# Kernel optimization log

Hardware: AMD Instinct MI355X
Metric: run time of the kernel (lower is better)

Reference implementation:

```python
import jax, jax.numpy as jnp
import numpy as np

D_MODEL = 256
NHEAD = 8
D_HEAD = D_MODEL // NHEAD


def setup_inputs() -> dict:
    key = jax.random.key(0)
    ks = jax.random.split(key, 5)
    s = 0.02
    return {
        "x": jax.random.normal(ks[0], (2, 4096, D_MODEL), dtype=jnp.float32),
        "source": jax.random.normal(ks[1], (2, 6144, D_MODEL), dtype=jnp.float32),
        "Wq": jax.random.normal(ks[2], (D_MODEL, D_MODEL), dtype=jnp.float32) * s,
        "Wk": jax.random.normal(ks[3], (D_MODEL, D_MODEL), dtype=jnp.float32) * s,
        "Wv": jax.random.normal(ks[4], (D_MODEL, D_MODEL), dtype=jnp.float32) * s,
    }


def reference(x, source, Wq, Wk, Wv):
    B, L1, D = x.shape
    L2 = source.shape[1]
    scale = D_HEAD ** (-0.5)
    # torch Linear: y = x @ W.T  (W is [out, in])
    q = (x @ Wq.T).reshape(B, L1, NHEAD, D_HEAD)
    k = (source @ Wk.T).reshape(B, L2, NHEAD, D_HEAD)
    v = (source @ Wv.T).reshape(B, L2, NHEAD, D_HEAD)
    # scores: [B, H, L1, L2]
    attn = jnp.einsum("bqhd,bkhd->bhqk", q, k) * scale
    attn = jax.nn.softmax(attn, axis=-1)
    out = jnp.einsum("bhqk,bkhd->bqhd", attn, v)
    return out.reshape(B, L1, D)
```

## Files before the change

### kernel.cpp

```cpp
#include <hip/hip_runtime.h>
#include <math.h>

#define B_   2
#define L1_  4096
#define L2_  6144
#define DM_  256
#define H_   8
#define DH_  32

typedef __bf16 bf16x8 __attribute__((ext_vector_type(8)));
typedef __bf16 bf16x4 __attribute__((ext_vector_type(4)));
typedef float floatx4 __attribute__((ext_vector_type(4)));

__device__ __forceinline__ bf16x8 ldb(const __bf16* p) { return *(const bf16x8*)p; }

__device__ __forceinline__ bf16x4 pack4(floatx4 v) {
    bf16x4 r;
    r[0] = (__bf16)v[0]; r[1] = (__bf16)v[1];
    r[2] = (__bf16)v[2]; r[3] = (__bf16)v[3];
    return r;
}

__device__ inline bf16x8 load_cvt8(const float* __restrict__ p, float scale) {
    float4 a = *(const float4*)p;
    float4 b = *(const float4*)(p + 4);
    bf16x8 r;
    r[0] = (__bf16)(a.x * scale); r[1] = (__bf16)(a.y * scale);
    r[2] = (__bf16)(a.z * scale); r[3] = (__bf16)(a.w * scale);
    r[4] = (__bf16)(b.x * scale); r[5] = (__bf16)(b.y * scale);
    r[6] = (__bf16)(b.z * scale); r[7] = (__bf16)(b.w * scale);
    return r;
}

__global__ __launch_bounds__(256) void cvtW_kernel(
    const float* __restrict__ wq, const float* __restrict__ wk,
    const float* __restrict__ wv, __bf16* __restrict__ o, float qscale)
{
    int i = blockIdx.x * 256 + threadIdx.x;
    int seg = i >> 14;
    int off = (i & 16383) * 4;
    const float* src = seg == 0 ? wq : (seg == 1 ? wk : wv);
    float s = seg == 0 ? qscale : 1.0f;
    float4 v = *(const float4*)(src + off);
    __bf16* dst = o + (size_t)seg * 65536 + off;
    dst[0] = (__bf16)(v.x * s); dst[1] = (__bf16)(v.y * s);
    dst[2] = (__bf16)(v.z * s); dst[3] = (__bf16)(v.w * s);
}

template<bool WBF>
__global__ __launch_bounds__(256, 2) void proj_kernel(
    const float* __restrict__ x, const float* __restrict__ src,
    const float* __restrict__ Wqf, const float* __restrict__ Wkf, const float* __restrict__ Wvf,
    const __bf16* __restrict__ Wbf,
    __bf16* __restrict__ qo, __bf16* __restrict__ ko, __bf16* __restrict__ vo,
    float qscale)
{
    const int y = blockIdx.y;
    const int L = (y == 0) ? L1_ : L2_;
    if (blockIdx.x * 32 >= B_ * L) return;

    const float*  X   = (y == 0) ? x : src;
    const float*  Wf  = (y == 0) ? Wqf : (y == 1 ? Wkf : Wvf);
    const __bf16* Wb  = Wbf + (size_t)y * 65536;
    __bf16*       out = (y == 0) ? qo : (y == 1 ? ko : vo);
    const float   ascale = (!WBF && y == 0) ? qscale : 1.0f;

    const int lane = threadIdx.x & 63;
    const int w    = threadIdx.x >> 6;
    const int g    = lane >> 4;
    const int c    = lane & 15;
    const int mb   = blockIdx.x * 32;
    const int b    = mb / L;
    const int lb   = mb - b * L;

    floatx4 acc[2][4];
#pragma unroll
    for (int s = 0; s < 2; s++)
#pragma unroll
        for (int n = 0; n < 4; n++) acc[s][n] = (floatx4){0.f, 0.f, 0.f, 0.f};

#pragma unroll
    for (int kc = 0; kc < 8; kc++) {
        bf16x8 xf0 = load_cvt8(X + (size_t)(mb + c) * DM_ + kc * 32 + g * 8, ascale);
        bf16x8 xf1 = load_cvt8(X + (size_t)(mb + 16 + c) * DM_ + kc * 32 + g * 8, ascale);
#pragma unroll
        for (int n = 0; n < 4; n++) {
            const int oc = w * 64 + n * 16 + c;
            bf16x8 wf;
            if (WBF) wf = ldb(Wb + (size_t)oc * DM_ + kc * 32 + g * 8);
            else     wf = load_cvt8(Wf + (size_t)oc * DM_ + kc * 32 + g * 8, 1.0f);
            if (y == 2) {
                acc[0][n] = __builtin_amdgcn_mfma_f32_16x16x32_bf16(xf0, wf, acc[0][n], 0, 0, 0);
                acc[1][n] = __builtin_amdgcn_mfma_f32_16x16x32_bf16(xf1, wf, acc[1][n], 0, 0, 0);
            } else {
                acc[0][n] = __builtin_amdgcn_mfma_f32_16x16x32_bf16(wf, xf0, acc[0][n], 0, 0, 0);
                acc[1][n] = __builtin_amdgcn_mfma_f32_16x16x32_bf16(wf, xf1, acc[1][n], 0, 0, 0);
            }
        }
    }

    const int bhb = b * H_;
    if (y == 2) {
#pragma unroll
        for (int s = 0; s < 2; s++)
#pragma unroll
            for (int n = 0; n < 4; n++) {
                int d = (n & 1) * 16 + c;
                int h = w * 2 + (n >> 1);
                int l = lb + s * 16 + g * 4;
                *(bf16x4*)(out + ((size_t)(bhb + h) * DH_ + d) * (size_t)L + l) = pack4(acc[s][n]);
            }
    } else {
#pragma unroll
        for (int s = 0; s < 2; s++)
#pragma unroll
            for (int n = 0; n < 4; n++) {
                int dlo = (n & 1) * 16 + g * 4;
                int h = w * 2 + (n >> 1);
                int l = lb + s * 16 + c;
                *(bf16x4*)(out + ((size_t)(bhb + h) * (size_t)L + l) * DH_ + dlo) = pack4(acc[s][n]);
            }
    }
}

__device__ __forceinline__ void attn_step(
    const bf16x8 (&qf)[4], const bf16x8 (&kf)[4], bf16x8 (&kfN)[4],
    const __bf16* __restrict__ knext,
    const __bf16* __restrict__ vb0, const __bf16* __restrict__ vb1, int kb,
    __bf16* __restrict__ Pw, int g, int c,
    float (&l)[4], floatx4 (&o)[4][2])
{
    bf16x8 vf0 = ldb(vb0 + kb);
    bf16x8 vf1 = ldb(vb1 + kb);
    bf16x8 vf2 = ldb(vb0 + kb + 32);
    bf16x8 vf3 = ldb(vb1 + kb + 32);
    kfN[0] = ldb(knext);
    kfN[1] = ldb(knext + 16 * DH_);
    kfN[2] = ldb(knext + 32 * DH_);
    kfN[3] = ldb(knext + 48 * DH_);

#pragma unroll
    for (int h = 0; h < 4; h++) {
        floatx4 s[4];
#pragma unroll
        for (int st = 0; st < 4; st++)
            s[st] = __builtin_amdgcn_mfma_f32_16x16x32_bf16(
                        kf[st], qf[h], (floatx4){0.f, 0.f, 0.f, 0.f}, 0, 0, 0);
#pragma unroll
        for (int st = 0; st < 4; st++) {
            float a0 = __builtin_amdgcn_exp2f(s[st][0]);
            float a1 = __builtin_amdgcn_exp2f(s[st][1]);
            float a2 = __builtin_amdgcn_exp2f(s[st][2]);
            float a3 = __builtin_amdgcn_exp2f(s[st][3]);
            l[h] += (a0 + a1) + (a2 + a3);
            bf16x4 pk;
            pk[0] = (__bf16)a0; pk[1] = (__bf16)a1;
            pk[2] = (__bf16)a2; pk[3] = (__bf16)a3;
            *(bf16x4*)(Pw + h * 1024 + ((st * 2 + (g >> 1)) * 16 + c) * 8 + (g & 1) * 4) = pk;
        }
    }

#pragma unroll
    for (int kc = 0; kc < 2; kc++) {
#pragma unroll
        for (int h = 0; h < 4; h++) {
            bf16x8 pa = *(const bf16x8*)(Pw + h * 1024 + ((kc * 4 + g) * 16 + c) * 8);
            o[h][0] = __builtin_amdgcn_mfma_f32_16x16x32_bf16(pa, kc ? vf2 : vf0, o[h][0], 0, 0, 0);
            o[h][1] = __builtin_amdgcn_mfma_f32_16x16x32_bf16(pa, kc ? vf3 : vf1, o[h][1], 0, 0, 0);
        }
    }
}

template<bool DIRECT>
__global__ __launch_bounds__(256, 2) void attn_kernel(
    const __bf16* __restrict__ Q, const __bf16* __restrict__ K,
    const __bf16* __restrict__ VT, float* __restrict__ out,
    float* __restrict__ Opart, float* __restrict__ Lpart, int klen)
{
    __shared__ __bf16 ldsP[4][4][1024];

    const int lane  = threadIdx.x & 63;
    const int w     = threadIdx.x >> 6;
    const int g     = lane >> 4;
    const int c     = lane & 15;
    const int qbase = blockIdx.x * 256 + w * 64;
    const int bh    = blockIdx.y;
    const int k0    = blockIdx.z * klen;

    bf16x8 qf[4];
#pragma unroll
    for (int h = 0; h < 4; h++)
        qf[h] = ldb(Q + ((size_t)bh * L1_ + qbase + h * 16 + c) * DH_ + g * 8);

    const __bf16* kbase = K  + (size_t)bh * L2_ * DH_ + (size_t)c * DH_ + g * 8;
    const __bf16* vb0   = VT + ((size_t)bh * DH_ + c)      * L2_ + g * 8;
    const __bf16* vb1   = VT + ((size_t)bh * DH_ + 16 + c) * L2_ + g * 8;
    __bf16* Pw = &ldsP[w][0][0];

    float l[4] = {0.f, 0.f, 0.f, 0.f};
    floatx4 o[4][2];
#pragma unroll
    for (int h = 0; h < 4; h++) { o[h][0] = (floatx4){0.f,0.f,0.f,0.f}; o[h][1] = (floatx4){0.f,0.f,0.f,0.f}; }

    bf16x8 kfA[4], kfB[4];
#pragma unroll
    for (int st = 0; st < 4; st++)
        kfA[st] = ldb(kbase + (size_t)(k0 + st * 16) * DH_);

    for (int t = 0; t < klen; t += 128) {
        int kb = k0 + t;
        attn_step(qf, kfA, kfB, kbase + (size_t)(kb + 64) * DH_,
                  vb0, vb1, kb, Pw, g, c, l, o);
        int nn = (t + 128 < klen) ? kb + 128 : k0;
        attn_step(qf, kfB, kfA, kbase + (size_t)nn * DH_,
                  vb0, vb1, kb + 64, Pw, g, c, l, o);
    }

#pragma unroll
    for (int h = 0; h < 4; h++) {
        l[h] += __shfl_xor(l[h], 16, 64);
        l[h] += __shfl_xor(l[h], 32, 64);
    }

    const int b  = bh / H_;
    const int hh = bh % H_;
    if (DIRECT) {
#pragma unroll
        for (int h = 0; h < 4; h++)
#pragma unroll
            for (int r = 0; r < 4; r++) {
                float lr  = __shfl(l[h], g * 4 + r, 64);
                float inv = 1.0f / lr;
                size_t base = ((size_t)(b * L1_ + qbase + h * 16 + g * 4 + r)) * DM_ + hh * DH_;
                out[base + c]      = o[h][0][r] * inv;
                out[base + 16 + c] = o[h][1][r] * inv;
            }
    } else {
        float* Op = Opart + (size_t)blockIdx.z * ((size_t)B_ * L1_ * DM_);
#pragma unroll
        for (int h = 0; h < 4; h++) {
#pragma unroll
            for (int r = 0; r < 4; r++) {
                size_t base = ((size_t)(b * L1_ + qbase + h * 16 + g * 4 + r)) * DM_ + hh * DH_;
                Op[base + c]      = o[h][0][r];
                Op[base + 16 + c] = o[h][1][r];
            }
            if (g == 0)
                Lpart[(size_t)blockIdx.z * ((size_t)B_ * H_ * L1_) +
                      (size_t)bh * L1_ + qbase + h * 16 + c] = l[h];
        }
    }
}

__global__ __launch_bounds__(256) void combine_kernel(
    const float* __restrict__ Opart, const float* __restrict__ Lpart,
    float* __restrict__ out, int split)
{
    int t   = blockIdx.x * 256 + threadIdx.x;
    int row = t >> 6;
    int col = (t & 63) * 4;
    int b   = row >> 12;
    int q   = row & (L1_ - 1);
    int bh  = b * H_ + (col >> 5);
    float4 a = {0.f, 0.f, 0.f, 0.f};
    float ls = 0.f;
    for (int z = 0; z < split; z++) {
        const float* Op = Opart + (size_t)z * ((size_t)B_ * L1_ * DM_);
        float4 v = *(const float4*)(Op + (size_t)row * DM_ + col);
        a.x += v.x; a.y += v.y; a.z += v.z; a.w += v.w;
        ls += Lpart[(size_t)z * ((size_t)B_ * H_ * L1_) + (size_t)bh * L1_ + q];
    }
    float inv = 1.0f / ls;
    float4 r; r.x = a.x * inv; r.y = a.y * inv; r.z = a.z * inv; r.w = a.w * inv;
    *(float4*)(out + (size_t)row * DM_ + col) = r;
}

extern "C" void kernel_launch(void* const* d_in, const int* in_sizes, int n_in,
                              void* d_out, int out_size, void* d_ws, size_t ws_size,
                              hipStream_t stream) {
    const float* x   = (const float*)d_in[0];
    const float* src = (const float*)d_in[1];
    const float* Wq  = (const float*)d_in[2];
    const float* Wk  = (const float*)d_in[3];
    const float* Wv  = (const float*)d_in[4];
    float* out = (float*)d_out;

    const float qscale = 1.4426950408889634f / sqrtf((float)DH_);

    const size_t nQ = (size_t)B_ * H_ * L1_ * DH_;
    const size_t nK = (size_t)B_ * H_ * L2_ * DH_;
    const size_t nW = 3 * 65536;
    const bool wbf_ok = ws_size >= (nW + nQ + 2 * nK) * sizeof(__bf16);

    __bf16 *wbf, *qws;
    if (wbf_ok) { wbf = (__bf16*)d_ws; qws = wbf + nW; }
    else        { wbf = nullptr;       qws = (__bf16*)d_ws; }
    __bf16* kws = qws + nQ;
    __bf16* vt  = kws + nK;

    size_t used = ((wbf_ok ? nW : 0) + nQ + 2 * nK) * sizeof(__bf16);
    used = (used + 255) & ~(size_t)255;
    const size_t oPartB = (size_t)B_ * L1_ * DM_ * 4;
    const size_t lPartB = (size_t)B_ * H_ * L1_ * 4;
    int split = 1;
    if      (ws_size >= used + 4 * (oPartB + lPartB)) split = 4;
    else if (ws_size >= used + 2 * (oPartB + lPartB)) split = 2;
    float* Opart = (float*)((char*)d_ws + used);
    float* Lpart = (float*)((char*)d_ws + used + (size_t)split * oPartB);

    if (wbf_ok) {
        cvtW_kernel<<<dim3(192), 256, 0, stream>>>(Wq, Wk, Wv, wbf, qscale);
        proj_kernel<true><<<dim3(384, 3), 256, 0, stream>>>(
            x, src, Wq, Wk, Wv, wbf, qws, kws, vt, qscale);
    } else {
        proj_kernel<false><<<dim3(384, 3), 256, 0, stream>>>(
            x, src, Wq, Wk, Wv, (const __bf16*)nullptr, qws, kws, vt, qscale);
    }

    if (split > 1) {
        attn_kernel<false><<<dim3(L1_ / 256, B_ * H_, split), 256, 0, stream>>>(
            qws, kws, vt, nullptr, Opart, Lpart, L2_ / split);
        combine_kernel<<<dim3(2048), 256, 0, stream>>>(Opart, Lpart, out, split);
    } else {
        attn_kernel<true><<<dim3(L1_ / 256, B_ * H_, 1), 256, 0, stream>>>(
            qws, kws, vt, out, nullptr, nullptr, L2_);
    }
}
```

Measured before the change: 188.9 us.

## Pre-convert inputs to bf16, stage V transpose via LDS, remap attention grid

A single conversion kernel now turns the weights plus x and source into bf16 buffers. The projection then reads bf16 directly, and its launch is flattened so blocks no longer return early. The V-transpose store goes through an LDS tile so each row is written with wide coalesced stores instead of scattered 8-byte writes. The attention grid becomes 1D with a swizzled block-to-work mapping, likely to place blocks across XCDs for better L2 locality. The cost is an extra pass that reads and writes the activations, and the bf16 staging buffers share workspace with the split partials.

```diff
diff --git a/kernel.cpp b/kernel.cpp
--- a/kernel.cpp
+++ b/kernel.cpp
@@ -21,55 +21,56 @@
     return r;
 }
 
-__device__ inline bf16x8 load_cvt8(const float* __restrict__ p, float scale) {
-    float4 a = *(const float4*)p;
-    float4 b = *(const float4*)(p + 4);
-    bf16x8 r;
-    r[0] = (__bf16)(a.x * scale); r[1] = (__bf16)(a.y * scale);
-    r[2] = (__bf16)(a.z * scale); r[3] = (__bf16)(a.w * scale);
-    r[4] = (__bf16)(b.x * scale); r[5] = (__bf16)(b.y * scale);
-    r[6] = (__bf16)(b.z * scale); r[7] = (__bf16)(b.w * scale);
-    return r;
-}
-
-__global__ __launch_bounds__(256) void cvtW_kernel(
+__global__ __launch_bounds__(256) void cvt_all(
     const float* __restrict__ wq, const float* __restrict__ wk,
-    const float* __restrict__ wv, __bf16* __restrict__ o, float qscale)
+    const float* __restrict__ wv, const float* __restrict__ x,
+    const float* __restrict__ src,
+    __bf16* __restrict__ wbf, __bf16* __restrict__ xbf, __bf16* __restrict__ sbf,
+    float qscale)
 {
     int i = blockIdx.x * 256 + threadIdx.x;
-    int seg = i >> 14;
-    int off = (i & 16383) * 4;
-    const float* src = seg == 0 ? wq : (seg == 1 ? wk : wv);
-    float s = seg == 0 ? qscale : 1.0f;
-    float4 v = *(const float4*)(src + off);
-    __bf16* dst = o + (size_t)seg * 65536 + off;
-    dst[0] = (__bf16)(v.x * s); dst[1] = (__bf16)(v.y * s);
-    dst[2] = (__bf16)(v.z * s); dst[3] = (__bf16)(v.w * s);
-}
-
-template<bool WBF>
-__global__ __launch_bounds__(256, 2) void proj_kernel(
-    const float* __restrict__ x, const float* __restrict__ src,
-    const float* __restrict__ Wqf, const float* __restrict__ Wkf, const float* __restrict__ Wvf,
+    const float* s; __bf16* d; float sc = 1.0f; size_t off;
+    if (i < 49152) {
+        int seg = i >> 14;
+        off = (size_t)(i & 16383) * 4;
+        s = seg == 0 ? wq : (seg == 1 ? wk : wv);
+        d = wbf + (size_t)seg * 65536;
+        if (seg == 0) sc = qscale;
+    } else if (i < 49152 + 524288) {
+        off = (size_t)(i - 49152) * 4; s = x; d = xbf;
+    } else {
+        off = (size_t)(i - 49152 - 524288) * 4; s = src; d = sbf;
+    }
+    float4 v = *(const float4*)(s + off);
+    bf16x4 r;
+    r[0] = (__bf16)(v.x * sc); r[1] = (__bf16)(v.y * sc);
+    r[2] = (__bf16)(v.z * sc); r[3] = (__bf16)(v.w * sc);
+    *(bf16x4*)(d + off) = r;
+}
+
+__global__ __launch_bounds__(256) void proj_kernel(
+    const __bf16* __restrict__ xbf, const __bf16* __restrict__ sbf,
     const __bf16* __restrict__ Wbf,
-    __bf16* __restrict__ qo, __bf16* __restrict__ ko, __bf16* __restrict__ vo,
-    float qscale)
-{
-    const int y = blockIdx.y;
+    __bf16* __restrict__ qo, __bf16* __restrict__ ko, __bf16* __restrict__ vo)
+{
+    __shared__ __bf16 ldsV[256 * 36];
+
+    const int bid = blockIdx.x;
+    int y, xb;
+    if      (bid < 256) { y = 0; xb = bid; }
+    else if (bid < 640) { y = 1; xb = bid - 256; }
+    else                { y = 2; xb = bid - 640; }
+
     const int L = (y == 0) ? L1_ : L2_;
-    if (blockIdx.x * 32 >= B_ * L) return;
-
-    const float*  X   = (y == 0) ? x : src;
-    const float*  Wf  = (y == 0) ? Wqf : (y == 1 ? Wkf : Wvf);
+    const __bf16* X   = (y == 0) ? xbf : sbf;
     const __bf16* Wb  = Wbf + (size_t)y * 65536;
     __bf16*       out = (y == 0) ? qo : (y == 1 ? ko : vo);
-    const float   ascale = (!WBF && y == 0) ? qscale : 1.0f;
 
     const int lane = threadIdx.x & 63;
     const int w    = threadIdx.x >> 6;
     const int g    = lane >> 4;
     const int c    = lane & 15;
-    const int mb   = blockIdx.x * 32;
+    const int mb   = xb * 32;
     const int b    = mb / L;
     const int lb   = mb - b * L;
 
@@ -81,14 +82,12 @@
 
 #pragma unroll
     for (int kc = 0; kc < 8; kc++) {
-        bf16x8 xf0 = load_cvt8(X + (size_t)(mb + c) * DM_ + kc * 32 + g * 8, ascale);
-        bf16x8 xf1 = load_cvt8(X + (size_t)(mb + 16 + c) * DM_ + kc * 32 + g * 8, ascale);
+        bf16x8 xf0 = ldb(X + (size_t)(mb + c) * DM_ + kc * 32 + g * 8);
+        bf16x8 xf1 = ldb(X + (size_t)(mb + 16 + c) * DM_ + kc * 32 + g * 8);
 #pragma unroll
         for (int n = 0; n < 4; n++) {
             const int oc = w * 64 + n * 16 + c;
-            bf16x8 wf;
-            if (WBF) wf = ldb(Wb + (size_t)oc * DM_ + kc * 32 + g * 8);
-            else     wf = load_cvt8(Wf + (size_t)oc * DM_ + kc * 32 + g * 8, 1.0f);
+            bf16x8 wf = ldb(Wb + (size_t)oc * DM_ + kc * 32 + g * 8);
             if (y == 2) {
                 acc[0][n] = __builtin_amdgcn_mfma_f32_16x16x32_bf16(xf0, wf, acc[0][n], 0, 0, 0);
                 acc[1][n] = __builtin_amdgcn_mfma_f32_16x16x32_bf16(xf1, wf, acc[1][n], 0, 0, 0);
@@ -105,11 +104,17 @@
         for (int s = 0; s < 2; s++)
 #pragma unroll
             for (int n = 0; n < 4; n++) {
-                int d = (n & 1) * 16 + c;
-                int h = w * 2 + (n >> 1);
-                int l = lb + s * 16 + g * 4;
-                *(bf16x4*)(out + ((size_t)(bhb + h) * DH_ + d) * (size_t)L + l) = pack4(acc[s][n]);
-            }
+                int dg = w * 64 + (n >> 1) * 32 + (n & 1) * 16 + c;
+                int ll = s * 16 + g * 4;
+                *(bf16x4*)(ldsV + (size_t)dg * 36 + ll) = pack4(acc[s][n]);
+            }
+        __syncthreads();
+        const int t = threadIdx.x;
+        const int h = t >> 5, d = t & 31;
+        __bf16* row = out + ((size_t)(bhb + h) * DH_ + d) * (size_t)L + lb;
+#pragma unroll
+        for (int j = 0; j < 4; j++)
+            *(bf16x8*)(row + j * 8) = *(const bf16x8*)(ldsV + (size_t)t * 36 + j * 8);
     } else {
 #pragma unroll
         for (int s = 0; s < 2; s++)
@@ -175,17 +180,22 @@
 __global__ __launch_bounds__(256, 2) void attn_kernel(
     const __bf16* __restrict__ Q, const __bf16* __restrict__ K,
     const __bf16* __restrict__ VT, float* __restrict__ out,
-    float* __restrict__ Opart, float* __restrict__ Lpart, int klen)
+    float* __restrict__ Opart, float* __restrict__ Lpart, int klen, int split)
 {
     __shared__ __bf16 ldsP[4][4][1024];
+
+    const int bid  = blockIdx.x;
+    const int work = (bid & 7) * (32 * split) + (bid >> 3);
+    const int xb   = work & 15;
+    const int bh   = (work >> 4) & 15;
+    const int z    = work >> 8;
 
     const int lane  = threadIdx.x & 63;
     const int w     = threadIdx.x >> 6;
     const int g     = lane >> 4;
     const int c     = lane & 15;
-    const int qbase = blockIdx.x * 256 + w * 64;
-    const int bh    = blockIdx.y;
-    const int k0    = blockIdx.z * klen;
+    const int qbase = xb * 256 + w * 64;
+    const int k0    = z * klen;
 
     bf16x8 qf[4];
 #pragma unroll
@@ -236,7 +246,7 @@
                 out[base + 16 + c] = o[h][1][r] * inv;
             }
     } else {
-        float* Op = Opart + (size_t)blockIdx.z * ((size_t)B_ * L1_ * DM_);
+        float* Op = Opart + (size_t)z * ((size_t)B_ * L1_ * DM_);
 #pragma unroll
         for (int h = 0; h < 4; h++) {
 #pragma unroll
@@ -246,7 +256,7 @@
                 Op[base + 16 + c] = o[h][1][r];
             }
             if (g == 0)
-                Lpart[(size_t)blockIdx.z * ((size_t)B_ * H_ * L1_) +
+                Lpart[(size_t)z * ((size_t)B_ * H_ * L1_) +
                       (size_t)bh * L1_ + qbase + h * 16 + c] = l[h];
         }
     }
@@ -287,42 +297,38 @@
 
     const float qscale = 1.4426950408889634f / sqrtf((float)DH_);
 
+    const size_t nW = 3 * 65536;
     const size_t nQ = (size_t)B_ * H_ * L1_ * DH_;
     const size_t nK = (size_t)B_ * H_ * L2_ * DH_;
-    const size_t nW = 3 * 65536;
-    const bool wbf_ok = ws_size >= (nW + nQ + 2 * nK) * sizeof(__bf16);
-
-    __bf16 *wbf, *qws;
-    if (wbf_ok) { wbf = (__bf16*)d_ws; qws = wbf + nW; }
-    else        { wbf = nullptr;       qws = (__bf16*)d_ws; }
+    const size_t nX = nQ;
+    const size_t nS = nK;
+
+    __bf16* wbf = (__bf16*)d_ws;
+    __bf16* qws = wbf + nW;
     __bf16* kws = qws + nQ;
     __bf16* vt  = kws + nK;
-
-    size_t used = ((wbf_ok ? nW : 0) + nQ + 2 * nK) * sizeof(__bf16);
-    used = (used + 255) & ~(size_t)255;
+    size_t unionOff = ((nW + nQ + 2 * nK) * sizeof(__bf16) + 255) & ~(size_t)255;
+    __bf16* xbf = (__bf16*)((char*)d_ws + unionOff);
+    __bf16* sbf = xbf + nX;
+
     const size_t oPartB = (size_t)B_ * L1_ * DM_ * 4;
     const size_t lPartB = (size_t)B_ * H_ * L1_ * 4;
+    const size_t avail  = ws_size > unionOff ? ws_size - unionOff : 0;
     int split = 1;
-    if      (ws_size >= used + 4 * (oPartB + lPartB)) split = 4;
-    else if (ws_size >= used + 2 * (oPartB + lPartB)) split = 2;
-    float* Opart = (float*)((char*)d_ws + used);
-    float* Lpart = (float*)((char*)d_ws + used + (size_t)split * oPartB);
-
-    if (wbf_ok) {
-        cvtW_kernel<<<dim3(192), 256, 0, stream>>>(Wq, Wk, Wv, wbf, qscale);
-        proj_kernel<true><<<dim3(384, 3), 256, 0, stream>>>(
-            x, src, Wq, Wk, Wv, wbf, qws, kws, vt, qscale);
-    } else {
-        proj_kernel<false><<<dim3(384, 3), 256, 0, stream>>>(
-            x, src, Wq, Wk, Wv, (const __bf16*)nullptr, qws, kws, vt, qscale);
-    }
+    if      (avail >= 4 * (oPartB + lPartB)) split = 4;
+    else if (avail >= 2 * (oPartB + lPartB)) split = 2;
+    float* Opart = (float*)((char*)d_ws + unionOff);
+    float* Lpart = (float*)((char*)d_ws + unionOff + (size_t)split * oPartB);
+
+    cvt_all<<<dim3(5312), 256, 0, stream>>>(Wq, Wk, Wv, x, src, wbf, xbf, sbf, qscale);
+    proj_kernel<<<dim3(1024), 256, 0, stream>>>(xbf, sbf, wbf, qws, kws, vt);
 
     if (split > 1) {
-        attn_kernel<false><<<dim3(L1_ / 256, B_ * H_, split), 256, 0, stream>>>(
-            qws, kws, vt, nullptr, Opart, Lpart, L2_ / split);
+        attn_kernel<false><<<dim3(256 * split), 256, 0, stream>>>(
+            qws, kws, vt, nullptr, Opart, Lpart, L2_ / split, split);
         combine_kernel<<<dim3(2048), 256, 0, stream>>>(Opart, Lpart, out, split);
     } else {
-        attn_kernel<true><<<dim3(L1_ / 256, B_ * H_, 1), 256, 0, stream>>>(
-            qws, kws, vt, out, nullptr, nullptr, L2_);
-    }
-}
+        attn_kernel<true><<<dim3(256), 256, 0, stream>>>(
+            qws, kws, vt, out, nullptr, nullptr, L2_, 1);
+    }
+}
```

New measurement: 188.9 us. No clear change (+0.0%).
